# Optimization experiments

Hardware: AMD Instinct MI355X
Metric: run time of the kernel (lower is better)

## Reference

```python
import jax, jax.numpy as jnp
import numpy as np
from jax import lax

B_, L_, D_MODEL, D_FF = 8, 1024, 512, 2048
D_STATE, D_CONV, EXPAND = 16, 4, 2
D_IN = EXPAND * D_MODEL
DT_RANK = (D_MODEL + 15) // 16  # 32


def _ln(x, g, b, eps=1e-5):
    m = jnp.mean(x, -1, keepdims=True)
    v = jnp.var(x, -1, keepdims=True)
    return (x - m) / jnp.sqrt(v + eps) * g + b


def _selective_scan(u, dt, A, Bm, Cm, D):
    # u, dt: (B,L,d_in); Bm, Cm: (B,L,d_state); A: (d_in,d_state); D: (d_in,)
    def step(h, xs):
        dt_t, B_t, C_t, u_t = xs  # (B,d_in),(B,ds),(B,ds),(B,d_in)
        dA = jnp.exp(dt_t[..., None] * A)                       # (B,d_in,ds)
        h = dA * h + (dt_t * u_t)[..., None] * B_t[:, None, :]  # (B,d_in,ds)
        y = jnp.einsum('bds,bs->bd', h, C_t)
        return h, y

    h0 = jnp.zeros((u.shape[0], D_IN, D_STATE), u.dtype)
    xs = (dt.transpose(1, 0, 2), Bm.transpose(1, 0, 2),
          Cm.transpose(1, 0, 2), u.transpose(1, 0, 2))
    _, ys = lax.scan(step, h0, xs)           # (L,B,d_in)
    return ys.transpose(1, 0, 2) + u * D


def _mamba(x, in_w, conv_w, conv_b, xp_w, dtp_w, dtp_b, A_log, D, out_w):
    xz = x @ in_w.T                              # (B,L,2*d_in)
    xs, z = jnp.split(xz, 2, axis=-1)
    # causal depthwise conv1d over L
    xc = lax.conv_general_dilated(xs.transpose(0, 2, 1), conv_w, (1,),
                                  [(D_CONV - 1, 0)], feature_group_count=D_IN)
    xc = jax.nn.silu(xc + conv_b[None, :, None]).transpose(0, 2, 1)  # (B,L,d_in)
    x_dbl = xc @ xp_w.T
    dt, Bm, Cm = jnp.split(x_dbl, [DT_RANK, DT_RANK + D_STATE], axis=-1)
    dt = jax.nn.softplus(dt @ dtp_w.T + dtp_b)
    A = -jnp.exp(A_log)
    y = _selective_scan(xc, dt, A, Bm, Cm, D)
    y = y * jax.nn.silu(z)
    return y @ out_w.T


def _forward(x,
             in1_w, conv1d1_w, conv1d1_b, xp1_w, dtp1_w, dtp1_b, Alog1, D1, outp1_w,
             in2_w, conv1d2_w, conv1d2_b, xp2_w, dtp2_w, dtp2_b, Alog2, D2, outp2_w,
             c1_w, c1_b, c2_w, c2_b, ln1_g, ln1_b, ln2_g, ln2_b):
    x_res = x  # dropout is identity in eval
    fwd = _mamba(x, in1_w, conv1d1_w, conv1d1_b, xp1_w, dtp1_w, dtp1_b, Alog1, D1, outp1_w)
    bwd = _mamba(jnp.flip(x, 1), in2_w, conv1d2_w, conv1d2_b, xp2_w, dtp2_w, dtp2_b,
                 Alog2, D2, outp2_w)
    new_x = fwd + jnp.flip(bwd, 1)
    x = _ln(new_x + x_res, ln1_g, ln1_b)
    y = jax.nn.gelu(jnp.einsum('bld,fd->blf', x, c1_w[:, :, 0]) + c1_b, approximate=False)
    y = jnp.einsum('blf,df->bld', y, c2_w[:, :, 0]) + c2_b
    return _ln(x + y, ln2_g, ln2_b)


def setup_inputs() -> dict:
    key = jax.random.key(0)
    ks = iter(jax.random.split(key, 32))
    rn = lambda shape, s=0.02: jax.random.normal(next(ks), shape, jnp.float32) * s

    def mamba_params():
        return dict(in_w=rn((2 * D_IN, D_MODEL)), conv_w=rn((D_IN, 1, D_CONV)),
                    conv_b=rn((D_IN,)), xp_w=rn((DT_RANK + 2 * D_STATE, D_IN)),
                    dtp_w=rn((D_IN, DT_RANK)), dtp_b=rn((D_IN,)),
                    A_log=jnp.log(jnp.tile(jnp.arange(1., D_STATE + 1.), (D_IN, 1))).astype(jnp.float32),
                    D=jnp.ones((D_IN,), jnp.float32), out_w=rn((D_MODEL, D_IN)))

    m1, m2 = mamba_params(), mamba_params()
    return {
        'x': jax.random.normal(next(ks), (B_, L_, D_MODEL), jnp.float32),
        'in1_w': m1['in_w'], 'conv1d1_w': m1['conv_w'], 'conv1d1_b': m1['conv_b'],
        'xp1_w': m1['xp_w'], 'dtp1_w': m1['dtp_w'], 'dtp1_b': m1['dtp_b'],
        'Alog1': m1['A_log'], 'D1': m1['D'], 'outp1_w': m1['out_w'],
        'in2_w': m2['in_w'], 'conv1d2_w': m2['conv_w'], 'conv1d2_b': m2['conv_b'],
        'xp2_w': m2['xp_w'], 'dtp2_w': m2['dtp_w'], 'dtp2_b': m2['dtp_b'],
        'Alog2': m2['A_log'], 'D2': m2['D'], 'outp2_w': m2['out_w'],
        'c1_w': rn((D_FF, D_MODEL, 1)), 'c1_b': rn((D_FF,)),
        'c2_w': rn((D_MODEL, D_FF, 1)), 'c2_b': rn((D_MODEL,)),
        'ln1_g': jnp.ones((D_MODEL,), jnp.float32), 'ln1_b': jnp.zeros((D_MODEL,), jnp.float32),
        'ln2_g': jnp.ones((D_MODEL,), jnp.float32), 'ln2_b': jnp.zeros((D_MODEL,), jnp.float32),
    }


def reference(x,
              in1_w, conv1d1_w, conv1d1_b, xp1_w, dtp1_w, dtp1_b, Alog1, D1, outp1_w,
              in2_w, conv1d2_w, conv1d2_b, xp2_w, dtp2_w, dtp2_b, Alog2, D2, outp2_w,
              c1_w, c1_b, c2_w, c2_b, ln1_g, ln1_b, ln2_g, ln2_b):
    return _forward(x,
                    in1_w, conv1d1_w, conv1d1_b, xp1_w, dtp1_w, dtp1_b, Alog1, D1, outp1_w,
                    in2_w, conv1d2_w, conv1d2_b, xp2_w, dtp2_w, dtp2_b, Alog2, D2, outp2_w,
                    c1_w, c1_b, c2_w, c2_b, ln1_g, ln1_b, ln2_g, ln2_b)
```

## Files before the change

kernel.cpp:

```cpp
#include <hip/hip_runtime.h>
#include <hip/hip_bf16.h>
#include <math.h>

#define B_SZ 8
#define L_SZ 1024
#define DM 512
#define DFF 2048
#define DIN 1024
#define DSTATE 16
#define DTRANK 32
#define MROWS (B_SZ * L_SZ)
#define CH 256
#define NCH 4

typedef __hip_bfloat16 bf16;
typedef unsigned short u16;
using f32x4 = __attribute__((ext_vector_type(4))) float;
using bfrag = __attribute__((ext_vector_type(8))) short;

__device__ inline float ldf(const float* p, long i) { return p[i]; }
__device__ inline float ldf(const bf16* p, long i) {
  return __uint_as_float((unsigned)((const u16*)p)[i] << 16);
}
__device__ inline void stf(float* p, long i, float v) { p[i] = v; }
__device__ inline void stf(bf16* p, long i, float v) { p[i] = __float2bfloat16(v); }
__device__ inline float b2f(u16 x) {
  return __uint_as_float((unsigned)x << 16);
}
__device__ inline u16 f2b(float v) {
  union { bf16 h; u16 u; } c;
  c.h = __float2bfloat16(v);
  return c.u;
}

__device__ inline float fexp2(float x) {
  float r;
  asm("v_exp_f32 %0, %1" : "=v"(r) : "v"(x));
  return r;
}

typedef __attribute__((address_space(1))) const void g_void;
typedef __attribute__((address_space(3))) void l_void;
__device__ inline void gl_lds16(const void* g, void* l) {
  __builtin_amdgcn_global_load_lds((g_void*)g, (l_void*)l, 16, 0, 0);
}

__device__ inline float4 ld4f_bt(const float* p) { return *(const float4*)p; }
__device__ inline float4 ld4f_bt(const bf16* p) {
  ushort4 u = *(const ushort4*)p;
  float4 v;
  v.x = b2f(u.x); v.y = b2f(u.y); v.z = b2f(u.z); v.w = b2f(u.w);
  return v;
}

__device__ inline void ld16f(const float* p, uint4& lo, uint4& hi) {
  float4 a = *(const float4*)p, b = *(const float4*)(p + 4);
  float4 c = *(const float4*)(p + 8), d = *(const float4*)(p + 12);
  union { uint4 v; u16 s[8]; } L, H;
  L.s[0] = f2b(a.x); L.s[1] = f2b(a.y); L.s[2] = f2b(a.z); L.s[3] = f2b(a.w);
  L.s[4] = f2b(b.x); L.s[5] = f2b(b.y); L.s[6] = f2b(b.z); L.s[7] = f2b(b.w);
  H.s[0] = f2b(c.x); H.s[1] = f2b(c.y); H.s[2] = f2b(c.z); H.s[3] = f2b(c.w);
  H.s[4] = f2b(d.x); H.s[5] = f2b(d.y); H.s[6] = f2b(d.z); H.s[7] = f2b(d.w);
  lo = L.v; hi = H.v;
}

__device__ inline float dpp_add_r8(float x) {
  float r; asm("v_add_f32 %0, %1, %2 row_ror:8" : "=v"(r) : "v"(x), "v"(x)); return r;
}
__device__ inline float dpp_add_r4(float x) {
  float r; asm("v_add_f32 %0, %1, %2 row_ror:4" : "=v"(r) : "v"(x), "v"(x)); return r;
}
__device__ inline float dpp_add_r2(float x) {
  float r; asm("v_add_f32 %0, %1, %2 row_ror:2" : "=v"(r) : "v"(x), "v"(x)); return r;
}
__device__ inline float dpp_add_r1(float x) {
  float r; asm("v_add_f32 %0, %1, %2 row_ror:1" : "=v"(r) : "v"(x), "v"(x)); return r;
}
__device__ inline float row16_sum(float x) {
  return dpp_add_r1(dpp_add_r2(dpp_add_r4(dpp_add_r8(x))));
}

__device__ inline int flipL(int r) {
  int t = r & (L_SZ - 1);
  return (r - t) + (L_SZ - 1 - t);
}

__global__ __launch_bounds__(256) void cvt8_k(
    const float* s0, const float* s1, const float* s2, const float* s3,
    const float* s4, const float* s5, const float* s6, const float* s7,
    bf16* d0, bf16* d1, bf16* d2, bf16* d3,
    bf16* d4, bf16* d5, bf16* d6, bf16* d7) {
  int blk = blockIdx.x;
  const float* s; bf16* d; long off;
  if (blk < 2048)       { s = s0; d = d0; off = (long)blk * 256; }
  else if (blk < 4096)  { s = s1; d = d1; off = (long)(blk - 2048) * 256; }
  else if (blk < 6144)  { s = s2; d = d2; off = (long)(blk - 4096) * 256; }
  else if (blk < 8192)  { s = s3; d = d3; off = (long)(blk - 6144) * 256; }
  else if (blk < 10240) { s = s4; d = d4; off = (long)(blk - 8192) * 256; }
  else if (blk < 12288) { s = s5; d = d5; off = (long)(blk - 10240) * 256; }
  else if (blk < 16384) { s = s6; d = d6; off = (long)(blk - 12288) * 256; }
  else                  { s = s7; d = d7; off = (long)(blk - 16384) * 256; }
  off += threadIdx.x;
  d[off] = __float2bfloat16(s[off]);
}

constexpr int MEPI_STORE2 = 0;
constexpr int MEPI_GATE2 = 1;
constexpr int MEPI_BIAS_GELU = 2;
constexpr int MEPI_BIAS_RES = 3;

template <int EPI, typename TA, typename TO>
__global__ __launch_bounds__(256) void mgemm_k(
    const TA* __restrict__ Ab, int lda,
    const bf16* __restrict__ Wb, int ldw,
    TO* __restrict__ C, TO* __restrict__ C2, int ldc,
    const float* __restrict__ bias,
    const float* __restrict__ res,
    int K) {
  constexpr bool ABF = (sizeof(TA) == 2);
  __shared__ u16 Wsm[128][32];
  __shared__ u16 AsmL[ABF ? 128 : 1][32];
  __shared__ u16 AsmP[ABF ? 1 : 128][ABF ? 1 : 40];
  const int tid = threadIdx.x;
  const int m0 = blockIdx.y * 128;
  const int n0 = blockIdx.x * 128;

  const int srow4 = tid >> 2;
  const int q16 = tid & 3;
  const u16* Wg0 = (const u16*)Wb + (long)(n0 + srow4) * ldw + q16 * 8;
  const u16* Wg1 = (const u16*)Wb + (long)(n0 + 64 + srow4) * ldw + q16 * 8;
  char* WsmB = (char*)&Wsm[0][0] + (tid >> 6) * 1024;

  const u16* Ag0 = (const u16*)Ab + (long)(m0 + srow4) * lda + q16 * 8;
  const u16* Ag1 = (const u16*)Ab + (long)(m0 + 64 + srow4) * lda + q16 * 8;
  char* AsmB = (char*)&AsmL[0][0] + (tid >> 6) * 1024;

  const int srow = tid >> 1;
  const int scol = (tid & 1) * 16;
  const TA* Agf = Ab + (long)(m0 + srow) * lda + scol;

  const int lane = tid & 63, quad = lane >> 4, l16 = lane & 15;
  const int wid = tid >> 6;
  const int wm = (wid & 1) * 64, wn = (wid >> 1) * 64;

  f32x4 acc[4][4];
#pragma unroll
  for (int i = 0; i < 4; ++i)
#pragma unroll
    for (int j = 0; j < 4; ++j) acc[i][j] = {0.f, 0.f, 0.f, 0.f};

  for (int k0 = 0; k0 < K; k0 += 32) {
    uint4 av0, av1;
    if constexpr (!ABF) ld16f((const float*)(Agf + k0), av0, av1);
    __syncthreads();
    gl_lds16(Wg0 + k0, WsmB);
    gl_lds16(Wg1 + k0, WsmB + 4096);
    if constexpr (ABF) {
      gl_lds16(Ag0 + k0, AsmB);
      gl_lds16(Ag1 + k0, AsmB + 4096);
    } else {
      *(uint4*)&AsmP[srow][scol] = av0;
      *(uint4*)&AsmP[srow][scol + 8] = av1;
    }
    __syncthreads();
    bfrag a[4], b[4];
#pragma unroll
    for (int mi = 0; mi < 4; ++mi) {
      if constexpr (ABF)
        a[mi] = *(const bfrag*)&AsmL[wm + mi * 16 + l16][quad * 8];
      else
        a[mi] = *(const bfrag*)&AsmP[wm + mi * 16 + l16][quad * 8];
    }
#pragma unroll
    for (int ni = 0; ni < 4; ++ni)
      b[ni] = *(const bfrag*)&Wsm[wn + ni * 16 + l16][quad * 8];
#pragma unroll
    for (int mi = 0; mi < 4; ++mi)
#pragma unroll
      for (int ni = 0; ni < 4; ++ni)
        acc[mi][ni] = __builtin_amdgcn_mfma_f32_16x16x32_bf16(
            a[mi], b[ni], acc[mi][ni], 0, 0, 0);
  }

  const bool second = (n0 >= DIN);
#pragma unroll
  for (int mi = 0; mi < 4; ++mi)
#pragma unroll
    for (int ni = 0; ni < 4; ++ni)
#pragma unroll
      for (int r = 0; r < 4; ++r) {
        int row = m0 + wm + mi * 16 + quad * 4 + r;
        int col = n0 + wn + ni * 16 + l16;
        float v = acc[mi][ni][r];
        if (EPI == MEPI_STORE2) {
          if (second) stf(C2, (long)flipL(row) * ldc + (col - DIN), v);
          else stf(C, (long)row * ldc + col, v);
        } else if (EPI == MEPI_GATE2) {
          TO* T = second ? C2 : C;
          long oi = second ? ((long)flipL(row) * ldc + (col - DIN))
                           : ((long)row * ldc + col);
          float y = ldf((const bf16*)T, oi);
          float sz = v / (1.f + __expf(-v));
          stf(T, oi, y * sz);
        } else if (EPI == MEPI_BIAS_GELU) {
          long oi = (long)row * ldc + col;
          v += bias[col];
          v = 0.5f * v * (1.f + erff(v * 0.70710678118654752440f));
          stf(C, oi, v);
        } else if (EPI == MEPI_BIAS_RES) {
          long oi = (long)row * ldc + col;
          ((float*)C)[oi] = v + bias[col] + res[oi];
        }
      }
}

__global__ __launch_bounds__(256) void mmerge_k(
    const bf16* __restrict__ y1, const bf16* __restrict__ y2,
    const bf16* __restrict__ W1, const bf16* __restrict__ W2,
    const float* __restrict__ xres, float* __restrict__ newx) {
  __shared__ u16 AsmL[128][32];
  __shared__ u16 Wsm[128][32];
  const int tid = threadIdx.x;
  const int m0 = blockIdx.y * 128;
  const int n0 = blockIdx.x * 128;

  const int srow4 = tid >> 2;
  const int q16 = tid & 3;
  int r1a = m0 + srow4, r1b = m0 + 64 + srow4;
  int r2a = flipL(r1a), r2b = flipL(r1b);
  const u16* A1g0 = (const u16*)y1 + (long)r1a * DIN + q16 * 8;
  const u16* A1g1 = (const u16*)y1 + (long)r1b * DIN + q16 * 8;
  const u16* A2g0 = (const u16*)y2 + (long)r2a * DIN + q16 * 8;
  const u16* A2g1 = (const u16*)y2 + (long)r2b * DIN + q16 * 8;
  const u16* W1g0 = (const u16*)W1 + (long)(n0 + srow4) * DIN + q16 * 8;
  const u16* W1g1 = (const u16*)W1 + (long)(n0 + 64 + srow4) * DIN + q16 * 8;
  const u16* W2g0 = (const u16*)W2 + (long)(n0 + srow4) * DIN + q16 * 8;
  const u16* W2g1 = (const u16*)W2 + (long)(n0 + 64 + srow4) * DIN + q16 * 8;
  char* AsmB = (char*)&AsmL[0][0] + (tid >> 6) * 1024;
  char* WsmB = (char*)&Wsm[0][0] + (tid >> 6) * 1024;

  const int lane = tid & 63, quad = lane >> 4, l16 = lane & 15;
  const int wid = tid >> 6;
  const int wm = (wid & 1) * 64, wn = (wid >> 1) * 64;

  f32x4 acc[4][4];
#pragma unroll
  for (int i = 0; i < 4; ++i)
#pragma unroll
    for (int j = 0; j < 4; ++j) acc[i][j] = {0.f, 0.f, 0.f, 0.f};

  for (int k0 = 0; k0 < 2 * DIN; k0 += 32) {
    const bool ph2 = (k0 >= DIN);
    const int kk = k0 & (DIN - 1);
    const u16* a0 = ph2 ? A2g0 : A1g0;
    const u16* a1 = ph2 ? A2g1 : A1g1;
    const u16* w0 = ph2 ? W2g0 : W1g0;
    const u16* w1 = ph2 ? W2g1 : W1g1;
    __syncthreads();
    gl_lds16(a0 + kk, AsmB);
    gl_lds16(a1 + kk, AsmB + 4096);
    gl_lds16(w0 + kk, WsmB);
    gl_lds16(w1 + kk, WsmB + 4096);
    __syncthreads();
    bfrag a[4], b[4];
#pragma unroll
    for (int mi = 0; mi < 4; ++mi)
      a[mi] = *(const bfrag*)&AsmL[wm + mi * 16 + l16][quad * 8];
#pragma unroll
    for (int ni = 0; ni < 4; ++ni)
      b[ni] = *(const bfrag*)&Wsm[wn + ni * 16 + l16][quad * 8];
#pragma unroll
    for (int mi = 0; mi < 4; ++mi)
#pragma unroll
      for (int ni = 0; ni < 4; ++ni)
        acc[mi][ni] = __builtin_amdgcn_mfma_f32_16x16x32_bf16(
            a[mi], b[ni], acc[mi][ni], 0, 0, 0);
  }

#pragma unroll
  for (int mi = 0; mi < 4; ++mi)
#pragma unroll
    for (int ni = 0; ni < 4; ++ni)
#pragma unroll
      for (int r = 0; r < 4; ++r) {
        int row = m0 + wm + mi * 16 + quad * 4 + r;
        int col = n0 + wn + ni * 16 + l16;
        long oi = (long)row * DM + col;
        newx[oi] = acc[mi][ni][r] + xres[oi];
      }
}

constexpr int EPI_NONE = 0;
constexpr int EPI_SOFTPLUS_ROW = 1;

#define BM 64
#define BN 64
#define BKK 16

template <int EPI, typename TB, typename TO>
__global__ __launch_bounds__(256) void gemmBT_k(
    const float* __restrict__ A,
    const TB* __restrict__ B,
    TO* __restrict__ C, int N,
    const float* __restrict__ bias, int K) {
  __shared__ float As[BKK][BM + 4];
  __shared__ float Bs[BKK][BN + 4];
  const int tid = threadIdx.x;
  const int m0 = blockIdx.y * BM;
  const int n0 = blockIdx.x * BN;
  const int tx = tid & 15;
  const int ty = tid >> 4;
  const int lrow = tid >> 2;
  const int lcol = (tid & 3) * 4;
  const int kr = tid >> 4;
  const int nc = (tid & 15) * 4;

  const float* Arow = A + (long)(m0 + lrow) * K;

  float acc[4][4] = {};
  for (int k0 = 0; k0 < K; k0 += BKK) {
    float4 av = *(const float4*)(Arow + k0 + lcol);
    float4 bv = ld4f_bt(B + (long)(k0 + kr) * N + n0 + nc);
    As[lcol + 0][lrow] = av.x; As[lcol + 1][lrow] = av.y;
    As[lcol + 2][lrow] = av.z; As[lcol + 3][lrow] = av.w;
    Bs[kr][nc + 0] = bv.x; Bs[kr][nc + 1] = bv.y;
    Bs[kr][nc + 2] = bv.z; Bs[kr][nc + 3] = bv.w;
    __syncthreads();
#pragma unroll
    for (int k = 0; k < BKK; ++k) {
      float a[4], b[4];
#pragma unroll
      for (int i = 0; i < 4; ++i) a[i] = As[k][ty * 4 + i];
#pragma unroll
      for (int j = 0; j < 4; ++j) b[j] = Bs[k][tx * 4 + j];
#pragma unroll
      for (int i = 0; i < 4; ++i)
#pragma unroll
        for (int j = 0; j < 4; ++j) acc[i][j] += a[i] * b[j];
    }
    __syncthreads();
  }

#pragma unroll
  for (int i = 0; i < 4; ++i) {
    int r = m0 + ty * 4 + i;
#pragma unroll
    for (int j = 0; j < 4; ++j) {
      int c = n0 + tx * 4 + j;
      float v = acc[i][j];
      if (EPI == EPI_SOFTPLUS_ROW) {
        v += bias[r];
        v = (v > 20.f) ? v : log1pf(__expf(v));
      }
      stf(C, (long)r * N + c, v);
    }
  }
}

__global__ __launch_bounds__(256) void convT_k(
    const bf16* __restrict__ xs, const float* __restrict__ w,
    const float* __restrict__ b, bf16* __restrict__ xcT) {
  __shared__ u16 T[64][72];
  int c0 = blockIdx.x * 64;
  int r0 = blockIdx.y * 64;
  int tid = threadIdx.x;
  int tr = tid >> 2;
  int tc = (tid & 3) * 16;

  const u16* src = (const u16*)xs + (long)(r0 + tr) * DIN + c0 + tc;
  uint4 v0 = *(const uint4*)src;
  uint4 v1 = *(const uint4*)(src + 8);
  u16 tmp[16];
  *(uint4*)tmp = v0;
  *(uint4*)(tmp + 8) = v1;
#pragma unroll
  for (int j = 0; j < 16; ++j) T[tc + j][tr + 3] = tmp[j];
  bool head = (r0 & (L_SZ - 1)) == 0;
  if (tid < 12) {
    int hr = tid >> 2;
    int seg = (tid & 3) * 16;
    if (head) {
#pragma unroll
      for (int j = 0; j < 16; ++j) T[seg + j][hr] = 0;
    } else {
      const u16* hs = (const u16*)xs + (long)(r0 - 3 + hr) * DIN + c0 + seg;
      uint4 h0 = *(const uint4*)hs;
      uint4 h1 = *(const uint4*)(hs + 8);
      u16 ht[16];
      *(uint4*)ht = h0;
      *(uint4*)(ht + 8) = h1;
#pragma unroll
      for (int j = 0; j < 16; ++j) T[seg + j][hr] = ht[j];
    }
  }
  __syncthreads();

  int d = c0 + tr;
  float w0 = w[d * 4 + 0], w1 = w[d * 4 + 1], w2 = w[d * 4 + 2], w3 = w[d * 4 + 3];
  float bd = b[d];
  float X[19];
#pragma unroll
  for (int k = 0; k < 19; ++k) X[k] = b2f(T[tr][tc + k]);
  u16 o[16];
#pragma unroll
  for (int j = 0; j < 16; ++j) {
    float acc = bd + w0 * X[j] + w1 * X[j + 1] + w2 * X[j + 2] + w3 * X[j + 3];
    o[j] = f2b(acc / (1.f + __expf(-acc)));
  }
  u16* dst = (u16*)xcT + (long)d * MROWS + r0 + tc;
  *(uint4*)dst = *(uint4*)o;
  *(uint4*)(dst + 8) = *(uint4*)(o + 8);
}

__global__ __launch_bounds__(256, 4) void scan1_k(
    const u16* __restrict__ dtT1, const u16* __restrict__ dtT2,
    const u16* __restrict__ uT1, const u16* __restrict__ uT2,
    const float* __restrict__ xd1, const float* __restrict__ xd2,
    const float* __restrict__ Alog1, const float* __restrict__ Alog2,
    bf16* __restrict__ hl1, bf16* __restrict__ hl2,
    float* __restrict__ sd1, float* __restrict__ sd2) {
  int blk = blockIdx.x;
  int dblk = blk & 15;
  int r = blk >> 4;
  int c = r % 3; r /= 3;
  int b = r & 7;
  int dir = r >> 3;
  int tid = threadIdx.x;
  int s = tid & 15;
  int gi = tid >> 4;
  int d0 = dblk * 64 + gi * 4;
  const u16* dtT = dir ? dtT2 : dtT1;
  const u16* uT = dir ? uT2 : uT1;
  const float* xd = dir ? xd2 : xd1;
  const float* Alog = dir ? Alog2 : Alog1;
  bf16* hl = dir ? hl2 : hl1;
  float* sd = dir ? sd2 : sd1;

  float A2[4], h[4], sdt[4];
#pragma unroll
  for (int dd = 0; dd < 4; ++dd) {
    A2[dd] = -__expf(Alog[(d0 + dd) * DSTATE + s]) * 1.4426950408889634f;
    h[dd] = 0.f;
    sdt[dd] = 0.f;
  }
  long t0 = (long)b * L_SZ + c * CH;
  const u16* pdt = dtT + (long)d0 * MROWS + t0;
  const u16* pu = uT + (long)d0 * MROWS + t0;
  const float* pB = xd + (long)(DTRANK + s) * MROWS + t0;

  for (int g = 0; g < CH / 8; ++g) {
    union { uint4 v; u16 a[8]; } dt8[4], u8[4];
    union { float4 v[2]; float a[8]; } B8;
#pragma unroll
    for (int dd = 0; dd < 4; ++dd) {
      dt8[dd].v = *(const uint4*)(pdt + (long)dd * MROWS + g * 8);
      u8[dd].v = *(const uint4*)(pu + (long)dd * MROWS + g * 8);
    }
    B8.v[0] = *(const float4*)(pB + g * 8);
    B8.v[1] = *(const float4*)(pB + g * 8 + 4);
#pragma unroll
    for (int j = 0; j < 8; ++j) {
      float Bj = B8.a[j];
#pragma unroll
      for (int dd = 0; dd < 4; ++dd) {
        float dtv = b2f(dt8[dd].a[j]);
        float uv = b2f(u8[dd].a[j]);
        float da = fexp2(dtv * A2[dd]);
        h[dd] = da * h[dd] + (dtv * uv) * Bj;
        sdt[dd] += dtv;
      }
    }
  }
#pragma unroll
  for (int dd = 0; dd < 4; ++dd) {
    int ci = (b * 3 + c) * 1024 + d0 + dd;
    hl[(long)ci * 16 + s] = __float2bfloat16(h[dd]);
    if (s == 0) sd[ci] = sdt[dd];
  }
}

__global__ __launch_bounds__(256, 4) void scan2_k(
    const u16* __restrict__ dtT1, const u16* __restrict__ dtT2,
    const u16* __restrict__ uT1, const u16* __restrict__ uT2,
    const float* __restrict__ xd1, const float* __restrict__ xd2,
    const float* __restrict__ Alog1, const float* __restrict__ Alog2,
    const float* __restrict__ D1, const float* __restrict__ D2,
    const bf16* __restrict__ hl1, const bf16* __restrict__ hl2,
    const float* __restrict__ sd1, const float* __restrict__ sd2,
    bf16* __restrict__ y1, bf16* __restrict__ y2) {
  int blk = blockIdx.x;
  int dblk = blk & 15;
  int c = (blk >> 4) & 3;
  int b = (blk >> 6) & 7;
  int dir = blk >> 9;
  int tid = threadIdx.x;
  int s = tid & 15;
  int gi = tid >> 4;
  int d0 = dblk * 64 + gi * 4;
  const u16* dtT = dir ? dtT2 : dtT1;
  const u16* uT = dir ? uT2 : uT1;
  const float* xd = dir ? xd2 : xd1;
  const float* Alog = dir ? Alog2 : Alog1;
  const float* Dp = dir ? D2 : D1;
  const bf16* hl = dir ? hl2 : hl1;
  const float* sd = dir ? sd2 : sd1;
  bf16* out = dir ? y2 : y1;

  float A2[4], h[4], Dd[4];
#pragma unroll
  for (int dd = 0; dd < 4; ++dd) {
    A2[dd] = -__expf(Alog[(d0 + dd) * DSTATE + s]) * 1.4426950408889634f;
    Dd[dd] = Dp[d0 + dd];
    h[dd] = 0.f;
  }

  for (int cc = 0; cc < c; ++cc) {
#pragma unroll
    for (int dd = 0; dd < 4; ++dd) {
      int ci = (b * 3 + cc) * 1024 + d0 + dd;
      float P = fexp2(A2[dd] * sd[ci]);
      h[dd] = h[dd] * P + b2f(((const u16*)hl)[(long)ci * 16 + s]);
    }
  }

  long t0 = (long)b * L_SZ + c * CH;
  const u16* pdt = dtT + (long)d0 * MROWS + t0;
  const u16* pu = uT + (long)d0 * MROWS + t0;
  const float* pB = xd + (long)(DTRANK + s) * MROWS + t0;
  const float* pC = xd + (long)(DTRANK + DSTATE + s) * MROWS + t0;
  u16* outb = (u16*)out + (long)b * L_SZ * DIN + (long)c * CH * DIN + d0;

  for (int g = 0; g < CH / 8; ++g) {
    union { uint4 v; u16 a[8]; } dt8[4], u8[4];
    union { float4 v[2]; float a[8]; } B8, C8;
#pragma unroll
    for (int dd = 0; dd < 4; ++dd) {
      dt8[dd].v = *(const uint4*)(pdt + (long)dd * MROWS + g * 8);
      u8[dd].v = *(const uint4*)(pu + (long)dd * MROWS + g * 8);
    }
    B8.v[0] = *(const float4*)(pB + g * 8);
    B8.v[1] = *(const float4*)(pB + g * 8 + 4);
    C8.v[0] = *(const float4*)(pC + g * 8);
    C8.v[1] = *(const float4*)(pC + g * 8 + 4);
    u16* og = outb + (long)g * 8 * DIN;
#pragma unroll
    for (int j = 0; j < 8; ++j) {
      float Bj = B8.a[j];
      float Cj = C8.a[j];
      u16 o4[4];
#pragma unroll
      for (int dd = 0; dd < 4; ++dd) {
        float dtv = b2f(dt8[dd].a[j]);
        float uv = b2f(u8[dd].a[j]);
        float da = fexp2(dtv * A2[dd]);
        h[dd] = da * h[dd] + (dtv * uv) * Bj;
        float q = row16_sum(h[dd] * Cj);
        o4[dd] = f2b(q + Dd[dd] * uv);
      }
      if (s == 0) *(uint2*)(og + (long)j * DIN) = *(uint2*)o4;
    }
  }
}

__global__ __launch_bounds__(256) void ln_k(
    const float* __restrict__ xin, const float* __restrict__ g,
    const float* __restrict__ bb, float* __restrict__ out,
    bf16* __restrict__ outb) {
  int row = blockIdx.x;
  const float* p = xin + (long)row * DM;
  int tid = threadIdx.x;
  float x0 = p[tid], x1 = p[tid + 256];
  float sum = x0 + x1;
  float sq = x0 * x0 + x1 * x1;
#pragma unroll
  for (int o = 1; o < 64; o <<= 1) {
    sum += __shfl_xor(sum, o, 64);
    sq += __shfl_xor(sq, o, 64);
  }
  __shared__ float ssum[4], ssq[4];
  int wv = tid >> 6;
  if ((tid & 63) == 0) { ssum[wv] = sum; ssq[wv] = sq; }
  __syncthreads();
  sum = ssum[0] + ssum[1] + ssum[2] + ssum[3];
  sq = ssq[0] + ssq[1] + ssq[2] + ssq[3];
  float mean = sum * (1.f / DM);
  float var = sq * (1.f / DM) - mean * mean;
  float rstd = rsqrtf(var + 1e-5f);
  float v0 = (x0 - mean) * rstd * g[tid] + bb[tid];
  float v1 = (x1 - mean) * rstd * g[tid + 256] + bb[tid + 256];
  out[(long)row * DM + tid] = v0;
  out[(long)row * DM + tid + 256] = v1;
  if (outb) {
    stf(outb, (long)row * DM + tid, v0);
    stf(outb, (long)row * DM + tid + 256, v1);
  }
}

extern "C" void kernel_launch(void* const* d_in, const int* in_sizes, int n_in,
                              void* d_out, int out_size, void* d_ws, size_t ws_size,
                              hipStream_t stream) {
  const float* x = (const float*)d_in[0];
  const float* in1_w = (const float*)d_in[1];
  const float* conv1_w = (const float*)d_in[2];
  const float* conv1_b = (const float*)d_in[3];
  const float* xp1_w = (const float*)d_in[4];
  const float* dtp1_w = (const float*)d_in[5];
  const float* dtp1_b = (const float*)d_in[6];
  const float* Alog1 = (const float*)d_in[7];
  const float* D1 = (const float*)d_in[8];
  const float* outp1_w = (const float*)d_in[9];
  const float* in2_w = (const float*)d_in[10];
  const float* conv2_w = (const float*)d_in[11];
  const float* conv2_b = (const float*)d_in[12];
  const float* xp2_w = (const float*)d_in[13];
  const float* dtp2_w = (const float*)d_in[14];
  const float* dtp2_b = (const float*)d_in[15];
  const float* Alog2 = (const float*)d_in[16];
  const float* D2 = (const float*)d_in[17];
  const float* outp2_w = (const float*)d_in[18];
  const float* c1_w = (const float*)d_in[19];
  const float* c1_b = (const float*)d_in[20];
  const float* c2_w = (const float*)d_in[21];
  const float* c2_b = (const float*)d_in[22];
  const float* ln1_g = (const float*)d_in[23];
  const float* ln1_b = (const float*)d_in[24];
  const float* ln2_g = (const float*)d_in[25];
  const float* ln2_b = (const float*)d_in[26];

  const long MB = 1024L * 1024;
  char* wsb = (char*)d_ws;
  bf16* A = (bf16*)(wsb + 0 * MB);
  bf16* B = (bf16*)(wsb + 16 * MB);
  bf16* C = (bf16*)(wsb + 32 * MB);
  bf16* D = (bf16*)(wsb + 48 * MB);
  bf16* E = (bf16*)(wsb + 64 * MB);
  bf16* F = (bf16*)(wsb + 80 * MB);
  float* Bf = (float*)B;
  float* Cf = (float*)C;
  float* Af = (float*)A;
  bf16* ffn = C;

  char* ob = (char*)d_out;
  bf16* Wxs = (bf16*)(ob + 0 * MB);
  bf16* Wg = (bf16*)(ob + 2 * MB);
  bf16* o1b = (bf16*)(ob + 4 * MB);
  bf16* o2b = (bf16*)(ob + 5 * MB);
  bf16* c1b = (bf16*)(ob + 6 * MB);
  bf16* c2b = (bf16*)(ob + 8 * MB);
  float* xdT1 = (float*)(ob + 10 * MB);
  float* xdT2 = (float*)(ob + 12 * MB);
  float* sd1 = (float*)(ob + 14 * MB);
  float* sd2 = (float*)(ob + 14 * MB + 131072);
  bf16* hl1 = (bf16*)(ob + 14 * MB + 262144);
  bf16* hl2 = (bf16*)(ob + 15 * MB);

  const long HWN = (long)DIN * DM;

  dim3 blk(256);
  dim3 gP2(2 * DIN / 128, MROWS / 128);
  dim3 gM(DM / 128, MROWS / 128);
  dim3 gF(DFF / 128, MROWS / 128);
  dim3 gC(DIN / 64, MROWS / 64);
  dim3 gX(MROWS / BN, 64 / BM);
  dim3 gD(MROWS / BN, DIN / BM);

  cvt8_k<<<20480, blk, 0, stream>>>(
      in1_w, in2_w, in1_w + HWN, in2_w + HWN, outp1_w, outp2_w, c1_w, c2_w,
      Wxs, Wxs + HWN, Wg, Wg + HWN, o1b, o2b, c1b, c2b);

  mgemm_k<MEPI_STORE2, float, bf16><<<gP2, blk, 0, stream>>>(
      x, DM, Wxs, DM, A, D, DIN, nullptr, nullptr, DM);

  convT_k<<<gC, blk, 0, stream>>>(A, conv1_w, conv1_b, B);
  convT_k<<<gC, blk, 0, stream>>>(D, conv2_w, conv2_b, E);

  gemmBT_k<EPI_NONE, bf16, float><<<gX, blk, 0, stream>>>(
      xp1_w, B, xdT1, MROWS, nullptr, DIN);
  gemmBT_k<EPI_SOFTPLUS_ROW, float, bf16><<<gD, blk, 0, stream>>>(
      dtp1_w, xdT1, C, MROWS, dtp1_b, DTRANK);
  gemmBT_k<EPI_NONE, bf16, float><<<gX, blk, 0, stream>>>(
      xp2_w, E, xdT2, MROWS, nullptr, DIN);
  gemmBT_k<EPI_SOFTPLUS_ROW, float, bf16><<<gD, blk, 0, stream>>>(
      dtp2_w, xdT2, F, MROWS, dtp2_b, DTRANK);

  scan1_k<<<2 * 8 * 3 * 16, blk, 0, stream>>>(
      (const u16*)C, (const u16*)F, (const u16*)B, (const u16*)E,
      xdT1, xdT2, Alog1, Alog2, hl1, hl2, sd1, sd2);
  scan2_k<<<2 * 8 * 4 * 16, blk, 0, stream>>>(
      (const u16*)C, (const u16*)F, (const u16*)B, (const u16*)E,
      xdT1, xdT2, Alog1, Alog2, D1, D2, hl1, hl2, sd1, sd2, A, D);

  mgemm_k<MEPI_GATE2, float, bf16><<<gP2, blk, 0, stream>>>(
      x, DM, Wg, DM, A, D, DIN, nullptr, nullptr, DM);

  mmerge_k<<<gM, blk, 0, stream>>>(A, D, o1b, o2b, x, Cf);

  ln_k<<<MROWS, blk, 0, stream>>>(Cf, ln1_g, ln1_b, Bf, E);

  mgemm_k<MEPI_BIAS_GELU, bf16, bf16><<<gF, blk, 0, stream>>>(
      E, DM, c1b, DM, ffn, nullptr, DFF, c1_b, nullptr, DM);
  mgemm_k<MEPI_BIAS_RES, bf16, float><<<gM, blk, 0, stream>>>(
      ffn, DFF, c2b, DFF, Af, nullptr, DM, c2_b, Bf, DFF);

  ln_k<<<MROWS, blk, 0, stream>>>(Af, ln2_g, ln2_b, (float*)d_out, nullptr);
}
```

Baseline: 800.4 us.

## Split-K x_proj GEMMs for both directions into one atomic-accumulating kernel

Replaces the two separate x_proj GEMM launches, which had only MROWS/BN x 1 blocks each with K=1024 walked serially, with one kernel. It splits K into 8 chunks of 128 and covers both directions through blockIdx.z, so many more blocks run in parallel. Partial sums go to the output with float atomicAdd, which needs a memset to zero the output buffers first. The trade is atomic traffic, an extra memset, and a summation order that is no longer deterministic.

New measurement: 881.5 us. +10.1%, slower.

```diff
diff --git a/kernel.cpp b/kernel.cpp
--- a/kernel.cpp
+++ b/kernel.cpp
@@ -353,6 +353,65 @@
         v = (v > 20.f) ? v : log1pf(__expf(v));
       }
       stf(C, (long)r * N + c, v);
+    }
+  }
+}
+
+__global__ __launch_bounds__(256) void xprojs_k(
+    const float* __restrict__ A1, const bf16* __restrict__ B1,
+    float* __restrict__ C1,
+    const float* __restrict__ A2, const bf16* __restrict__ B2,
+    float* __restrict__ C2) {
+  __shared__ float As[BKK][BM + 4];
+  __shared__ float Bs[BKK][BN + 4];
+  const int tid = threadIdx.x;
+  const int n0 = blockIdx.x * BN;
+  const int kbeg = blockIdx.y * 128;
+  const int dir = blockIdx.z;
+  const float* A = dir ? A2 : A1;
+  const bf16* Bm = dir ? B2 : B1;
+  float* C = dir ? C2 : C1;
+  const int N = MROWS, K = DIN;
+  const int tx = tid & 15;
+  const int ty = tid >> 4;
+  const int lrow = tid >> 2;
+  const int lcol = (tid & 3) * 4;
+  const int kr = tid >> 4;
+  const int nc = (tid & 15) * 4;
+
+  const float* Arow = A + (long)lrow * K;
+
+  float acc[4][4] = {};
+  for (int k0 = kbeg; k0 < kbeg + 128; k0 += BKK) {
+    float4 av = *(const float4*)(Arow + k0 + lcol);
+    float4 bv = ld4f_bt(Bm + (long)(k0 + kr) * N + n0 + nc);
+    As[lcol + 0][lrow] = av.x; As[lcol + 1][lrow] = av.y;
+    As[lcol + 2][lrow] = av.z; As[lcol + 3][lrow] = av.w;
+    Bs[kr][nc + 0] = bv.x; Bs[kr][nc + 1] = bv.y;
+    Bs[kr][nc + 2] = bv.z; Bs[kr][nc + 3] = bv.w;
+    __syncthreads();
+#pragma unroll
+    for (int k = 0; k < BKK; ++k) {
+      float a[4], b[4];
+#pragma unroll
+      for (int i = 0; i < 4; ++i) a[i] = As[k][ty * 4 + i];
+#pragma unroll
+      for (int j = 0; j < 4; ++j) b[j] = Bs[k][tx * 4 + j];
+#pragma unroll
+      for (int i = 0; i < 4; ++i)
+#pragma unroll
+        for (int j = 0; j < 4; ++j) acc[i][j] += a[i] * b[j];
+    }
+    __syncthreads();
+  }
+
+#pragma unroll
+  for (int i = 0; i < 4; ++i) {
+    int r = ty * 4 + i;
+#pragma unroll
+    for (int j = 0; j < 4; ++j) {
+      int c = n0 + tx * 4 + j;
+      atomicAdd(&C[(long)r * N + c], acc[i][j]);
     }
   }
 }
@@ -661,12 +720,13 @@
   dim3 gM(DM / 128, MROWS / 128);
   dim3 gF(DFF / 128, MROWS / 128);
   dim3 gC(DIN / 64, MROWS / 64);
-  dim3 gX(MROWS / BN, 64 / BM);
+  dim3 gXs(MROWS / BN, DIN / 128, 2);
   dim3 gD(MROWS / BN, DIN / BM);
 
   cvt8_k<<<20480, blk, 0, stream>>>(
       in1_w, in2_w, in1_w + HWN, in2_w + HWN, outp1_w, outp2_w, c1_w, c2_w,
       Wxs, Wxs + HWN, Wg, Wg + HWN, o1b, o2b, c1b, c2b);
+  hipMemsetAsync(xdT1, 0, 4 * MB, stream);
 
   mgemm_k<MEPI_STORE2, float, bf16><<<gP2, blk, 0, stream>>>(
       x, DM, Wxs, DM, A, D, DIN, nullptr, nullptr, DM);
@@ -674,12 +734,10 @@
   convT_k<<<gC, blk, 0, stream>>>(A, conv1_w, conv1_b, B);
   convT_k<<<gC, blk, 0, stream>>>(D, conv2_w, conv2_b, E);
 
-  gemmBT_k<EPI_NONE, bf16, float><<<gX, blk, 0, stream>>>(
-      xp1_w, B, xdT1, MROWS, nullptr, DIN);
+  xprojs_k<<<gXs, blk, 0, stream>>>(xp1_w, B, xdT1, xp2_w, E, xdT2);
+
   gemmBT_k<EPI_SOFTPLUS_ROW, float, bf16><<<gD, blk, 0, stream>>>(
       dtp1_w, xdT1, C, MROWS, dtp1_b, DTRANK);
-  gemmBT_k<EPI_NONE, bf16, float><<<gX, blk, 0, stream>>>(
-      xp2_w, E, xdT2, MROWS, nullptr, DIN);
   gemmBT_k<EPI_SOFTPLUS_ROW, float, bf16><<<gD, blk, 0, stream>>>(
       dtp2_w, xdT2, F, MROWS, dtp2_b, DTRANK);
 
```
